# Optimization experiments

Measured on AMD Instinct MI355X. Metric: run time of the kernel, lower is better.

## Reference

```python
import jax, jax.numpy as jnp
import numpy as np


def setup_inputs() -> dict:
    key = jax.random.key(0)
    ks = jax.random.split(key, 20)
    B, T, E, U, D, O = 64, 2048, 256, 256, 256, 32000
    s = lambda k, shp, fan: (jax.random.normal(k, shp, jnp.float32) * (1.0 / np.sqrt(fan)))
    return {
        'inputs': jax.random.normal(ks[0], (B, D), jnp.float32),
        'stm': jax.random.normal(ks[1], (B, U), jnp.float32),
        'x_seq': jax.random.normal(ks[2], (B, T, E), jnp.float32),
        'V_a': s(ks[3], (U + E,), U + E),
        'W_a': s(ks[4], (U + E, U + E), U + E),
        'W_r': s(ks[5], (D, U), D), 'U_r': s(ks[6], (U, U), U), 'C_r': s(ks[7], (E, U), E), 'b_r': jnp.zeros((U,), jnp.float32),
        'W_z': s(ks[8], (D, U), D), 'U_z': s(ks[9], (U, U), U), 'C_z': s(ks[10], (E, U), E), 'b_z': jnp.zeros((U,), jnp.float32),
        'W_p': s(ks[11], (D, U), D), 'U_p': s(ks[12], (U, U), U), 'C_p': s(ks[13], (E, U), E), 'b_p': jnp.zeros((U,), jnp.float32),
        'W_o': s(ks[14], (D, O), D), 'U_o': s(ks[15], (U, O), U), 'C_o': s(ks[16], (E, O), E), 'b_o': jnp.zeros((O,), jnp.float32),
    }


def reference(inputs, stm, x_seq, V_a, W_a,
              W_r, U_r, C_r, b_r,
              W_z, U_z, C_z, b_z,
              W_p, U_p, C_p, b_p,
              W_o, U_o, C_o, b_o):
    B, T, E = x_seq.shape
    U = stm.shape[-1]
    # Bahdanau additive attention: concat repeated state with encoder seq
    _stm = jnp.broadcast_to(stm[:, None, :], (B, T, U))          # [B,T,U]
    cat = jnp.concatenate([_stm, x_seq], axis=-1)                 # [B,T,U+E]
    et = jnp.einsum('btc,c->bt', jnp.tanh(jnp.einsum('btc,cd->btd', cat, W_a)), V_a)
    at = jax.nn.softmax(et, axis=1)                               # exp / sum over T
    context = jnp.einsum('bt,bte->be', at, x_seq)                 # [B,E]
    # GRU-style gates conditioned on input, previous state, and context
    rt = jax.nn.sigmoid(inputs @ W_r + stm @ U_r + context @ C_r + b_r)
    zt = jax.nn.sigmoid(inputs @ W_z + stm @ U_z + context @ C_z + b_z)
    s_tp = jnp.tanh(inputs @ W_p + (rt * stm) @ U_p + context @ C_p + b_p)
    st = (1.0 - zt) * stm + zt * s_tp                             # new state [B,U]
    output = jax.nn.softmax(inputs @ W_o + stm @ U_o + context @ C_o + b_o, axis=-1)  # [B,O]
    return output, st
```

## Files before the change

kernel.cpp:

```cpp
#include <hip/hip_runtime.h>
#include <hip/hip_bf16.h>

#define B_ 64
#define T_ 2048
#define E_ 256
#define U_ 256
#define O_ 32000
#define UE_ 512

typedef __attribute__((ext_vector_type(8))) short bf16x8;
typedef __attribute__((ext_vector_type(4))) float f32x4;

__device__ __forceinline__ unsigned short f2bf(float f){
  __hip_bfloat16 h = __float2bfloat16(f);
  return __builtin_bit_cast(unsigned short, h);
}
__device__ __forceinline__ unsigned pk2bf(float a, float b){
  return (unsigned)f2bf(a) | ((unsigned)f2bf(b) << 16);
}
__device__ __forceinline__ bf16x8 pack8(const float* v0, const float* v1){
  float4 x = *(const float4*)v0;
  float4 y = *(const float4*)v1;
  uint4 pk;
  pk.x = pk2bf(x.x, x.y); pk.y = pk2bf(x.z, x.w);
  pk.z = pk2bf(y.x, y.y); pk.w = pk2bf(y.z, y.w);
  return __builtin_bit_cast(bf16x8, pk);
}
__device__ __forceinline__ float ftanh(float x){
  float e = __expf(2.0f*x);
  return 1.0f - 2.0f/(e + 1.0f);
}
__device__ __forceinline__ float fsig(float x){
  return 1.0f/(1.0f + __expf(-x));
}

__global__ __launch_bounds__(256)
void prep_kernel(const float* __restrict__ Wa, const float* __restrict__ stm,
                 unsigned short* __restrict__ bpack, float* __restrict__ sp){
  if (blockIdx.x < 64){
    int idx = blockIdx.x*256 + threadIdx.x;
    int n = idx & 511;
    int ktg = idx >> 9;
    int erow = ktg * 8;
    unsigned short o[8];
#pragma unroll
    for (int i = 0; i < 8; ++i)
      o[i] = f2bf(Wa[(256 + erow + i)*512 + n]);
    uint4 v;
    v.x = (unsigned)o[0] | ((unsigned)o[1] << 16);
    v.y = (unsigned)o[2] | ((unsigned)o[3] << 16);
    v.z = (unsigned)o[4] | ((unsigned)o[5] << 16);
    v.w = (unsigned)o[6] | ((unsigned)o[7] << 16);
    ((uint4*)bpack)[idx] = v;
  } else {
    int tid = threadIdx.x;
    int w = tid >> 6, l = tid & 63, c = l & 15, g = l >> 4;
    int n0 = (blockIdx.x - 64)*64 + w*16;
    f32x4 zero = {0.f,0.f,0.f,0.f};
    f32x4 acc[4];
#pragma unroll
    for (int mt = 0; mt < 4; ++mt) acc[mt] = zero;
#pragma unroll
    for (int ks = 0; ks < 8; ++ks){
      int kg = ks*32 + 8*g;
      bf16x8 a[4];
#pragma unroll
      for (int mt = 0; mt < 4; ++mt){
        const float* ap = stm + (mt*16 + c)*256 + kg;
        a[mt] = pack8(ap, ap + 4);
      }
      const float* bpt = Wa + (size_t)kg*512 + n0 + c;
      float bv[8];
#pragma unroll
      for (int i = 0; i < 8; ++i) bv[i] = bpt[(size_t)i*512];
      uint4 pk;
      pk.x = pk2bf(bv[0], bv[1]); pk.y = pk2bf(bv[2], bv[3]);
      pk.z = pk2bf(bv[4], bv[5]); pk.w = pk2bf(bv[6], bv[7]);
      bf16x8 bfr = __builtin_bit_cast(bf16x8, pk);
#pragma unroll
      for (int mt = 0; mt < 4; ++mt)
        acc[mt] = __builtin_amdgcn_mfma_f32_16x16x32_bf16(a[mt], bfr, acc[mt], 0, 0, 0);
    }
#pragma unroll
    for (int mt = 0; mt < 4; ++mt)
#pragma unroll
      for (int r = 0; r < 4; ++r){
        int m = mt*16 + 4*g + r;
        sp[m*512 + n0 + c] = acc[mt][r];
      }
  }
}

__global__ __launch_bounds__(512, 4)
void et_flash_kernel(const float* __restrict__ xseq, const unsigned short* __restrict__ bpack,
                     const float* __restrict__ va, const float* __restrict__ sp,
                     float* __restrict__ msbuf, float* __restrict__ uctxp){
  __shared__ __align__(16) uint4 sA4[2048];
  __shared__ float sVa[512];
  __shared__ float sSp[512];
  __shared__ float sEt[8][64];
  __shared__ float sE[64];
  int tid = threadIdx.x;
  int w = tid >> 6, l = tid & 63, c = l & 15, g = l >> 4;
  int m0 = blockIdx.x * 64;
  int b  = m0 >> 11;

  const float4* x4 = (const float4*)xseq + (size_t)m0 * 64;
  uint2* sA2 = (uint2*)sA4;
#pragma unroll
  for (int i = 0; i < 8; ++i){
    int p = i*512 + tid;
    int row = p >> 6, kq = p & 63;
    float4 v = x4[row*64 + kq];
    uint2 u;
    u.x = pk2bf(v.x, v.y);
    u.y = pk2bf(v.z, v.w);
    int s = ((row>>4)*8 + (kq>>3))*64 + ((kq>>1)&3)*16 + (row&15);
    sA2[(s ^ ((s>>4)&7))*2 + (kq&1)] = u;
  }
  sVa[tid] = va[tid];
  sSp[tid] = sp[b*512 + tid];
  __syncthreads();

  f32x4 zero = {0.f, 0.f, 0.f, 0.f};
  f32x4 acc[4][4];
#pragma unroll
  for (int mt = 0; mt < 4; ++mt)
#pragma unroll
    for (int tc = 0; tc < 4; ++tc) acc[mt][tc] = zero;

  const bf16x8* bp = (const bf16x8*)bpack;
#pragma unroll
  for (int ks = 0; ks < 8; ++ks){
    bf16x8 aw[4], bx[4];
    int bbase = (ks*4 + g)*512 + w*64 + c;
#pragma unroll
    for (int mt = 0; mt < 4; ++mt)
      aw[mt] = bp[bbase + mt*16];
#pragma unroll
    for (int tc = 0; tc < 4; ++tc){
      int idx = (tc*8 + ks)*64 + l;
      bx[tc] = *(const bf16x8*)&sA4[idx ^ ((idx>>4)&7)];
    }
    __builtin_amdgcn_s_setprio(1);
#pragma unroll
    for (int mt = 0; mt < 4; ++mt)
#pragma unroll
      for (int tc = 0; tc < 4; ++tc)
        acc[mt][tc] = __builtin_amdgcn_mfma_f32_16x16x32_bf16(aw[mt], bx[tc], acc[mt][tc], 0, 0, 0);
    __builtin_amdgcn_s_setprio(0);
  }

  float p[4] = {0.f, 0.f, 0.f, 0.f};
#pragma unroll
  for (int mt = 0; mt < 4; ++mt){
    int nb = w*64 + mt*16 + 4*g;
    float4 vav = *(const float4*)&sVa[nb];
    float4 spv = *(const float4*)&sSp[nb];
#pragma unroll
    for (int tc = 0; tc < 4; ++tc){
#pragma unroll
      for (int r = 0; r < 4; ++r){
        float vv = acc[mt][tc][r] + ((const float*)&spv)[r];
        p[tc] += ((const float*)&vav)[r] * ftanh(vv);
      }
    }
  }
#pragma unroll
  for (int tc = 0; tc < 4; ++tc){
    p[tc] += __shfl_xor(p[tc], 16, 64);
    p[tc] += __shfl_xor(p[tc], 32, 64);
  }
  if (l < 16){
#pragma unroll
    for (int tc = 0; tc < 4; ++tc)
      sEt[w][tc*16 + c] = p[tc];
  }
  __syncthreads();

  if (tid < 64){
    float e = 0.f;
#pragma unroll
    for (int ww = 0; ww < 8; ++ww) e += sEt[ww][tid];
    float m = e;
#pragma unroll
    for (int off = 1; off < 64; off <<= 1) m = fmaxf(m, __shfl_xor(m, off, 64));
    float ex = __expf(e - m);
    float s = ex;
#pragma unroll
    for (int off = 1; off < 64; off <<= 1) s += __shfl_xor(s, off, 64);
    sE[tid] = ex;
    if (tid == 0){
      msbuf[blockIdx.x*2]     = m;
      msbuf[blockIdx.x*2 + 1] = s;
    }
  }
  __syncthreads();

  {
    int e = tid & 255, th = tid >> 8;
    int ks = e >> 5, gg = (e >> 3) & 3, ii = e & 7;
    const unsigned short* sU = (const unsigned short*)sA4;
    float a0 = 0.f;
#pragma unroll
    for (int tt = 0; tt < 32; ++tt){
      int t = th*32 + tt;
      int mt = t >> 4, cc = t & 15;
      int slt = (mt*8 + ks)*64 + gg*16 + cc;
      unsigned short hv = sU[(size_t)(slt ^ ((slt>>4)&7))*8 + ii];
      float xv = __builtin_bit_cast(float, ((unsigned)hv) << 16);
      a0 += sE[t] * xv;
    }
    uctxp[((size_t)blockIdx.x*2 + th)*256 + e] = a0;
  }
}

__global__ void ctx_x1_kernel(const float* __restrict__ msbuf, const float* __restrict__ uctxp,
                              const float* __restrict__ inputs, const float* __restrict__ stm,
                              unsigned short* __restrict__ X1bf){
  int b = blockIdx.x, e = threadIdx.x;
  float M = -INFINITY;
#pragma unroll 4
  for (int j = 0; j < 32; ++j) M = fmaxf(M, msbuf[(32*b + j)*2]);
  float S = 0.f;
  float acc = 0.f;
#pragma unroll 4
  for (int j = 0; j < 32; ++j){
    float wj = __expf(msbuf[(32*b + j)*2] - M);
    S += msbuf[(32*b + j)*2 + 1] * wj;
    size_t base = ((size_t)(32*b + j)*2)*256 + e;
    acc += (uctxp[base] + uctxp[base + 256]) * wj;
  }
  float ctx = acc / S;
  X1bf[b*768 + e]        = f2bf(inputs[b*256 + e]);
  X1bf[b*768 + 256 + e]  = f2bf(stm[b*256 + e]);
  X1bf[b*768 + 512 + e]  = f2bf(ctx);
}

__global__ __launch_bounds__(256)
void gates1_kernel(const unsigned short* __restrict__ X1bf, const float* __restrict__ stm,
                   const float* __restrict__ Wr, const float* __restrict__ Ur,
                   const float* __restrict__ Cr, const float* __restrict__ brr,
                   const float* __restrict__ Wz, const float* __restrict__ Uz,
                   const float* __restrict__ Cz, const float* __restrict__ bzz,
                   const float* __restrict__ Wp, const float* __restrict__ Cp,
                   const float* __restrict__ bpp,
                   float* __restrict__ rs, float* __restrict__ ztb, float* __restrict__ pic){
  int tid = threadIdx.x;
  int w = tid >> 6, l = tid & 63, c = l & 15, g = l >> 4;
  int n0 = blockIdx.x*64 + w*16;
  int gate = n0 >> 8;
  int col0 = n0 & 255;
  const float* W0; const float* W1; const float* W2; const float* bias;
  if (gate == 0){ W0 = Wr; W1 = Ur; W2 = Cr; bias = brr; }
  else if (gate == 1){ W0 = Wz; W1 = Uz; W2 = Cz; bias = bzz; }
  else { W0 = Wp; W1 = nullptr; W2 = Cp; bias = bpp; }

  f32x4 zero = {0.f,0.f,0.f,0.f};
  f32x4 acc[4];
#pragma unroll
  for (int mt = 0; mt < 4; ++mt) acc[mt] = zero;

#pragma unroll
  for (int ph = 0; ph < 3; ++ph){
    const float* src = (ph == 0) ? W0 : (ph == 1) ? W1 : W2;
    if (src == nullptr) continue;
#pragma unroll
    for (int ks = 0; ks < 8; ++ks){
      int kg = ks*32 + 8*g;
      bf16x8 a[4];
#pragma unroll
      for (int mt = 0; mt < 4; ++mt)
        a[mt] = *(const bf16x8*)&X1bf[(mt*16 + c)*768 + ph*256 + kg];
      const float* bpt = src + (size_t)kg*256 + col0 + c;
      float bv[8];
#pragma unroll
      for (int i = 0; i < 8; ++i) bv[i] = bpt[(size_t)i*256];
      uint4 pk;
      pk.x = pk2bf(bv[0], bv[1]); pk.y = pk2bf(bv[2], bv[3]);
      pk.z = pk2bf(bv[4], bv[5]); pk.w = pk2bf(bv[6], bv[7]);
      bf16x8 bfr = __builtin_bit_cast(bf16x8, pk);
#pragma unroll
      for (int mt = 0; mt < 4; ++mt)
        acc[mt] = __builtin_amdgcn_mfma_f32_16x16x32_bf16(a[mt], bfr, acc[mt], 0, 0, 0);
    }
  }

  int n = col0 + c;
  float bi = bias[n];
#pragma unroll
  for (int mt = 0; mt < 4; ++mt)
#pragma unroll
    for (int r = 0; r < 4; ++r){
      int m = mt*16 + 4*g + r;
      float pre = acc[mt][r] + bi;
      if (gate == 0)      rs[m*256 + n]  = fsig(pre) * stm[m*256 + n];
      else if (gate == 1) ztb[m*256 + n] = fsig(pre);
      else                pic[m*256 + n] = pre;
    }
}

__global__ __launch_bounds__(256)
void gates2_kernel(const float* __restrict__ rs, const float* __restrict__ Up,
                   const float* __restrict__ pic, const float* __restrict__ ztb,
                   const float* __restrict__ stm, float* __restrict__ stout){
  int tid = threadIdx.x;
  int w = tid >> 6, l = tid & 63, c = l & 15, g = l >> 4;
  int n0 = blockIdx.x*64 + w*16;
  f32x4 zero = {0.f,0.f,0.f,0.f};
  f32x4 acc[4];
#pragma unroll
  for (int mt = 0; mt < 4; ++mt) acc[mt] = zero;
#pragma unroll
  for (int ks = 0; ks < 8; ++ks){
    int kg = ks*32 + 8*g;
    bf16x8 a[4];
#pragma unroll
    for (int mt = 0; mt < 4; ++mt){
      const float* ap = rs + (mt*16 + c)*256 + kg;
      a[mt] = pack8(ap, ap + 4);
    }
    const float* bpt = Up + (size_t)kg*256 + n0 + c;
    float bv[8];
#pragma unroll
    for (int i = 0; i < 8; ++i) bv[i] = bpt[(size_t)i*256];
    uint4 pk;
    pk.x = pk2bf(bv[0], bv[1]); pk.y = pk2bf(bv[2], bv[3]);
    pk.z = pk2bf(bv[4], bv[5]); pk.w = pk2bf(bv[6], bv[7]);
    bf16x8 bfr = __builtin_bit_cast(bf16x8, pk);
#pragma unroll
    for (int mt = 0; mt < 4; ++mt)
      acc[mt] = __builtin_amdgcn_mfma_f32_16x16x32_bf16(a[mt], bfr, acc[mt], 0, 0, 0);
  }
#pragma unroll
  for (int mt = 0; mt < 4; ++mt)
#pragma unroll
    for (int r = 0; r < 4; ++r){
      int m = mt*16 + 4*g + r;
      int o = m*256 + n0 + c;
      float ap = pic[o] + acc[mt][r];
      float z = ztb[o];
      stout[o] = (1.f - z)*stm[o] + z*ftanh(ap);
    }
}

__global__ __launch_bounds__(512)
void logits_mfma_kernel(const unsigned short* __restrict__ X1bf,
                        const float* __restrict__ Wo, const float* __restrict__ Uo,
                        const float* __restrict__ Co, const float* __restrict__ boo,
                        float* __restrict__ outl, float* __restrict__ part2){
  __shared__ float sAcc[16][4][64];
  __shared__ float sMx[4][64];
  __shared__ float sSx[4][64];
  int tid = threadIdx.x;
  int w = tid >> 6, l = tid & 63, c = l & 15, g = l >> 4;
  int wc = w & 3;
  int kh = w >> 2;
  int n0 = blockIdx.x*64 + wc*16;
  f32x4 zero = {0.f,0.f,0.f,0.f};
  f32x4 acc[4];
#pragma unroll
  for (int mt = 0; mt < 4; ++mt) acc[mt] = zero;

#pragma unroll
  for (int ph = 0; ph < 3; ++ph){
    const float* src = (ph == 0) ? Wo : (ph == 1) ? Uo : Co;
#pragma unroll
    for (int kss = 0; kss < 4; ++kss){
      int ks = 2*kss + kh;
      int kg = ph*256 + ks*32 + 8*g;
      bf16x8 a[4];
#pragma unroll
      for (int mt = 0; mt < 4; ++mt)
        a[mt] = *(const bf16x8*)&X1bf[(mt*16 + c)*768 + kg];
      const float* bpt = src + (size_t)(ks*32 + 8*g)*32000 + n0 + c;
      float bv[8];
#pragma unroll
      for (int i = 0; i < 8; ++i) bv[i] = bpt[(size_t)i*32000];
      uint4 pk;
      pk.x = pk2bf(bv[0], bv[1]);
      pk.y = pk2bf(bv[2], bv[3]);
      pk.z = pk2bf(bv[4], bv[5]);
      pk.w = pk2bf(bv[6], bv[7]);
      bf16x8 bfr = __builtin_bit_cast(bf16x8, pk);
#pragma unroll
      for (int mt = 0; mt < 4; ++mt)
        acc[mt] = __builtin_amdgcn_mfma_f32_16x16x32_bf16(a[mt], bfr, acc[mt], 0, 0, 0);
    }
  }

  if (kh == 1){
#pragma unroll
    for (int mt = 0; mt < 4; ++mt)
#pragma unroll
      for (int r = 0; r < 4; ++r)
        sAcc[mt*4 + r][wc][l] = acc[mt][r];
  }
  __syncthreads();

  bool active = (kh == 0);
  float vv[4][4];
  if (active){
    float bias = boo[n0 + c];
#pragma unroll
    for (int mt = 0; mt < 4; ++mt)
#pragma unroll
      for (int r = 0; r < 4; ++r){
        int m = mt*16 + 4*g + r;
        vv[mt][r] = acc[mt][r] + sAcc[mt*4 + r][wc][l] + bias;
        outl[(size_t)m*32000 + n0 + c] = vv[mt][r];
      }
    float mx[4][4];
#pragma unroll
    for (int mt = 0; mt < 4; ++mt)
#pragma unroll
      for (int r = 0; r < 4; ++r) mx[mt][r] = vv[mt][r];
#pragma unroll
    for (int mask = 1; mask < 16; mask <<= 1)
#pragma unroll
      for (int mt = 0; mt < 4; ++mt)
#pragma unroll
        for (int r = 0; r < 4; ++r)
          mx[mt][r] = fmaxf(mx[mt][r], __shfl_xor(mx[mt][r], mask, 64));
    if (c == 0)
#pragma unroll
      for (int mt = 0; mt < 4; ++mt)
#pragma unroll
        for (int r = 0; r < 4; ++r)
          sMx[wc][mt*16 + 4*g + r] = mx[mt][r];
  }
  __syncthreads();
  if (active){
    float sx[4][4];
#pragma unroll
    for (int mt = 0; mt < 4; ++mt)
#pragma unroll
      for (int r = 0; r < 4; ++r){
        int row = mt*16 + 4*g + r;
        float M = fmaxf(fmaxf(sMx[0][row], sMx[1][row]), fmaxf(sMx[2][row], sMx[3][row]));
        sx[mt][r] = __expf(vv[mt][r] - M);
      }
#pragma unroll
    for (int mask = 1; mask < 16; mask <<= 1)
#pragma unroll
      for (int mt = 0; mt < 4; ++mt)
#pragma unroll
        for (int r = 0; r < 4; ++r)
          sx[mt][r] += __shfl_xor(sx[mt][r], mask, 64);
    if (c == 0)
#pragma unroll
      for (int mt = 0; mt < 4; ++mt)
#pragma unroll
        for (int r = 0; r < 4; ++r)
          sSx[wc][mt*16 + 4*g + r] = sx[mt][r];
  }
  __syncthreads();
  if (tid < 64){
    int row = tid;
    float M = fmaxf(fmaxf(sMx[0][row], sMx[1][row]), fmaxf(sMx[2][row], sMx[3][row]));
    float S = sSx[0][row] + sSx[1][row] + sSx[2][row] + sSx[3][row];
    part2[((size_t)blockIdx.x*64 + row)*2]     = M;
    part2[((size_t)blockIdx.x*64 + row)*2 + 1] = S;
  }
}

__global__ __launch_bounds__(512)
void sm_norm_kernel(float* __restrict__ logits, const float* __restrict__ part2){
  __shared__ float red[8];
  __shared__ float red2[8];
  __shared__ float sMS[2];
  int bid = blockIdx.x;
  int b = bid >> 3, ch = bid & 7;
  int base = b*32000 + ch*4000;
  int tid = threadIdx.x;

  float M = -INFINITY, S = 0.f;
  if (tid < 500){
    M = part2[((size_t)tid*64 + b)*2];
    S = part2[((size_t)tid*64 + b)*2 + 1];
  }
  float m1 = M;
#pragma unroll
  for (int off = 1; off < 64; off <<= 1) m1 = fmaxf(m1, __shfl_xor(m1, off, 64));
  int wv = tid >> 6;
  if ((tid & 63) == 0) red[wv] = m1;
  __syncthreads();
  float Mg = red[0];
#pragma unroll
  for (int i = 1; i < 8; ++i) Mg = fmaxf(Mg, red[i]);
  float s1 = (tid < 500) ? S * __expf(M - Mg) : 0.f;
#pragma unroll
  for (int off = 1; off < 64; off <<= 1) s1 += __shfl_xor(s1, off, 64);
  if ((tid & 63) == 0) red2[wv] = s1;
  __syncthreads();
  if (tid == 0){
    float St = 0.f;
#pragma unroll
    for (int i = 0; i < 8; ++i) St += red2[i];
    sMS[0] = Mg;
    sMS[1] = 1.0f / St;
  }
  __syncthreads();
  float Mf = sMS[0];
  float inv = sMS[1];
#pragma unroll
  for (int i = 0; i < 8; ++i){
    int idx = i*512 + tid;
    if (idx < 4000){
      int o = base + idx;
      logits[o] = __expf(logits[o] - Mf) * inv;
    }
  }
}

extern "C" void kernel_launch(void* const* d_in, const int* in_sizes, int n_in,
                              void* d_out, int out_size, void* d_ws, size_t ws_size,
                              hipStream_t stream) {
  const float* inputs = (const float*)d_in[0];
  const float* stm    = (const float*)d_in[1];
  const float* xseq   = (const float*)d_in[2];
  const float* Va     = (const float*)d_in[3];
  const float* Wa     = (const float*)d_in[4];
  const float* Wr = (const float*)d_in[5];
  const float* Ur = (const float*)d_in[6];
  const float* Cr = (const float*)d_in[7];
  const float* br = (const float*)d_in[8];
  const float* Wz = (const float*)d_in[9];
  const float* Uz = (const float*)d_in[10];
  const float* Cz = (const float*)d_in[11];
  const float* bz = (const float*)d_in[12];
  const float* Wp = (const float*)d_in[13];
  const float* Up = (const float*)d_in[14];
  const float* Cp = (const float*)d_in[15];
  const float* bp = (const float*)d_in[16];
  const float* Wo = (const float*)d_in[17];
  const float* Uo = (const float*)d_in[18];
  const float* Co = (const float*)d_in[19];
  const float* bo = (const float*)d_in[20];

  float* out   = (float*)d_out;
  float* stout = out + (size_t)B_*O_;

  float* wsf = (float*)d_ws;
  unsigned short* bpack = (unsigned short*)d_ws;
  float* sp    = wsf + 65536;
  float* msbuf = wsf + 98304;
  float* uctxp = wsf + 102400;
  float* part2 = wsf + 102400;
  unsigned short* X1bf = (unsigned short*)(wsf + 1150976);
  float* rs    = wsf + 1176576;
  float* ztb   = wsf + 1192960;
  float* pic   = wsf + 1209344;

  prep_kernel<<<72, 256, 0, stream>>>(Wa, stm, bpack, sp);
  et_flash_kernel<<<2048, 512, 0, stream>>>(xseq, bpack, Va, sp, msbuf, uctxp);
  ctx_x1_kernel<<<64, 256, 0, stream>>>(msbuf, uctxp, inputs, stm, X1bf);
  gates1_kernel<<<12, 256, 0, stream>>>(X1bf, stm, Wr, Ur, Cr, br,
                                        Wz, Uz, Cz, bz, Wp, Cp, bp,
                                        rs, ztb, pic);
  gates2_kernel<<<4, 256, 0, stream>>>(rs, Up, pic, ztb, stm, stout);
  logits_mfma_kernel<<<500, 512, 0, stream>>>(X1bf, Wo, Uo, Co, bo, out, part2);
  sm_norm_kernel<<<512, 512, 0, stream>>>(out, part2);
}
```

Before: 161.3 us.

## Overlap context-independent logits GEMM with attention kernel via extra blocks

Splits the output-logits GEMM so the inputs·W_o and stm·U_o parts, which don't depend on the attention context, run as extra blocks appended to the attention kernel launch. The final logits kernel now only multiplies the context by C_o and adds the stored partial sums. The bf16 packing of inputs and stm moves into the prep kernel so it is ready earlier. The goal is to hide logits weight streaming behind the x_seq pass. The cost is writing and reading back an extra full-size partial-logit buffer, plus contention between the two workloads.

```diff
diff --git a/kernel.cpp b/kernel.cpp
--- a/kernel.cpp
+++ b/kernel.cpp
@@ -36,7 +36,9 @@
 
 __global__ __launch_bounds__(256)
 void prep_kernel(const float* __restrict__ Wa, const float* __restrict__ stm,
-                 unsigned short* __restrict__ bpack, float* __restrict__ sp){
+                 const float* __restrict__ inputs,
+                 unsigned short* __restrict__ bpack, float* __restrict__ sp,
+                 unsigned short* __restrict__ X1bf){
   if (blockIdx.x < 64){
     int idx = blockIdx.x*256 + threadIdx.x;
     int n = idx & 511;
@@ -52,7 +54,7 @@
     v.z = (unsigned)o[4] | ((unsigned)o[5] << 16);
     v.w = (unsigned)o[6] | ((unsigned)o[7] << 16);
     ((uint4*)bpack)[idx] = v;
-  } else {
+  } else if (blockIdx.x < 72){
     int tid = threadIdx.x;
     int w = tid >> 6, l = tid & 63, c = l & 15, g = l >> 4;
     int n0 = (blockIdx.x - 64)*64 + w*16;
@@ -88,19 +90,84 @@
         int m = mt*16 + 4*g + r;
         sp[m*512 + n0 + c] = acc[mt][r];
       }
+  } else {
+    for (int j = threadIdx.x; j < 32768; j += 256){
+      int b = j >> 9, col = j & 511;
+      float v = (col < 256) ? inputs[b*256 + col] : stm[b*256 + col - 256];
+      X1bf[b*768 + col] = f2bf(v);
+    }
   }
 }
 
 __global__ __launch_bounds__(512, 4)
 void et_flash_kernel(const float* __restrict__ xseq, const unsigned short* __restrict__ bpack,
                      const float* __restrict__ va, const float* __restrict__ sp,
-                     float* __restrict__ msbuf, float* __restrict__ uctxp){
+                     float* __restrict__ msbuf, float* __restrict__ uctxp,
+                     const unsigned short* __restrict__ X1bf,
+                     const float* __restrict__ Wo, const float* __restrict__ Uo,
+                     float* __restrict__ lpart){
   __shared__ __align__(16) uint4 sA4[2048];
   __shared__ float sVa[512];
   __shared__ float sSp[512];
   __shared__ float sEt[8][64];
   __shared__ float sE[64];
   int tid = threadIdx.x;
+
+  if (blockIdx.x >= 2048){
+    int pb = blockIdx.x - 2048;
+    int w = tid >> 6, l = tid & 63, c = l & 15, g = l >> 4;
+    int wc = w & 3;
+    int kh = w >> 2;
+    int n0 = pb*64 + wc*16;
+    float* sAcc = (float*)sA4;
+    f32x4 zero = {0.f,0.f,0.f,0.f};
+    f32x4 acc[4];
+#pragma unroll
+    for (int mt = 0; mt < 4; ++mt) acc[mt] = zero;
+#pragma unroll
+    for (int ph = 0; ph < 2; ++ph){
+      const float* src = (ph == 0) ? Wo : Uo;
+#pragma unroll
+      for (int kss = 0; kss < 4; ++kss){
+        int ks = 2*kss + kh;
+        int kg = ph*256 + ks*32 + 8*g;
+        bf16x8 a[4];
+#pragma unroll
+        for (int mt = 0; mt < 4; ++mt)
+          a[mt] = *(const bf16x8*)&X1bf[(mt*16 + c)*768 + kg];
+        const float* bpt = src + (size_t)(ks*32 + 8*g)*32000 + n0 + c;
+        float bv[8];
+#pragma unroll
+        for (int i = 0; i < 8; ++i) bv[i] = bpt[(size_t)i*32000];
+        uint4 pk;
+        pk.x = pk2bf(bv[0], bv[1]); pk.y = pk2bf(bv[2], bv[3]);
+        pk.z = pk2bf(bv[4], bv[5]); pk.w = pk2bf(bv[6], bv[7]);
+        bf16x8 bfr = __builtin_bit_cast(bf16x8, pk);
+#pragma unroll
+        for (int mt = 0; mt < 4; ++mt)
+          acc[mt] = __builtin_amdgcn_mfma_f32_16x16x32_bf16(a[mt], bfr, acc[mt], 0, 0, 0);
+      }
+    }
+    if (kh == 1){
+#pragma unroll
+      for (int mt = 0; mt < 4; ++mt)
+#pragma unroll
+        for (int r = 0; r < 4; ++r)
+          sAcc[(mt*4 + r)*256 + wc*64 + l] = acc[mt][r];
+    }
+    __syncthreads();
+    if (kh == 0){
+#pragma unroll
+      for (int mt = 0; mt < 4; ++mt)
+#pragma unroll
+        for (int r = 0; r < 4; ++r){
+          int m = mt*16 + 4*g + r;
+          lpart[(size_t)m*32000 + n0 + c] = acc[mt][r] + sAcc[(mt*4 + r)*256 + wc*64 + l];
+        }
+    }
+    return;
+  }
+
   int w = tid >> 6, l = tid & 63, c = l & 15, g = l >> 4;
   int m0 = blockIdx.x * 64;
   int b  = m0 >> 11;
@@ -216,7 +283,6 @@
 }
 
 __global__ void ctx_x1_kernel(const float* __restrict__ msbuf, const float* __restrict__ uctxp,
-                              const float* __restrict__ inputs, const float* __restrict__ stm,
                               unsigned short* __restrict__ X1bf){
   int b = blockIdx.x, e = threadIdx.x;
   float M = -INFINITY;
@@ -232,9 +298,7 @@
     acc += (uctxp[base] + uctxp[base + 256]) * wj;
   }
   float ctx = acc / S;
-  X1bf[b*768 + e]        = f2bf(inputs[b*256 + e]);
-  X1bf[b*768 + 256 + e]  = f2bf(stm[b*256 + e]);
-  X1bf[b*768 + 512 + e]  = f2bf(ctx);
+  X1bf[b*768 + 512 + e] = f2bf(ctx);
 }
 
 __global__ __launch_bounds__(256)
@@ -345,10 +409,10 @@
 }
 
 __global__ __launch_bounds__(512)
-void logits_mfma_kernel(const unsigned short* __restrict__ X1bf,
-                        const float* __restrict__ Wo, const float* __restrict__ Uo,
-                        const float* __restrict__ Co, const float* __restrict__ boo,
-                        float* __restrict__ outl, float* __restrict__ part2){
+void logits_final_kernel(const unsigned short* __restrict__ X1bf,
+                         const float* __restrict__ Co, const float* __restrict__ lpart,
+                         const float* __restrict__ boo,
+                         float* __restrict__ outl, float* __restrict__ part2){
   __shared__ float sAcc[16][4][64];
   __shared__ float sMx[4][64];
   __shared__ float sSx[4][64];
@@ -363,30 +427,26 @@
   for (int mt = 0; mt < 4; ++mt) acc[mt] = zero;
 
 #pragma unroll
-  for (int ph = 0; ph < 3; ++ph){
-    const float* src = (ph == 0) ? Wo : (ph == 1) ? Uo : Co;
-#pragma unroll
-    for (int kss = 0; kss < 4; ++kss){
-      int ks = 2*kss + kh;
-      int kg = ph*256 + ks*32 + 8*g;
-      bf16x8 a[4];
-#pragma unroll
-      for (int mt = 0; mt < 4; ++mt)
-        a[mt] = *(const bf16x8*)&X1bf[(mt*16 + c)*768 + kg];
-      const float* bpt = src + (size_t)(ks*32 + 8*g)*32000 + n0 + c;
-      float bv[8];
-#pragma unroll
-      for (int i = 0; i < 8; ++i) bv[i] = bpt[(size_t)i*32000];
-      uint4 pk;
-      pk.x = pk2bf(bv[0], bv[1]);
-      pk.y = pk2bf(bv[2], bv[3]);
-      pk.z = pk2bf(bv[4], bv[5]);
-      pk.w = pk2bf(bv[6], bv[7]);
-      bf16x8 bfr = __builtin_bit_cast(bf16x8, pk);
-#pragma unroll
-      for (int mt = 0; mt < 4; ++mt)
-        acc[mt] = __builtin_amdgcn_mfma_f32_16x16x32_bf16(a[mt], bfr, acc[mt], 0, 0, 0);
-    }
+  for (int kss = 0; kss < 4; ++kss){
+    int ks = 2*kss + kh;
+    int kg = 512 + ks*32 + 8*g;
+    bf16x8 a[4];
+#pragma unroll
+    for (int mt = 0; mt < 4; ++mt)
+      a[mt] = *(const bf16x8*)&X1bf[(mt*16 + c)*768 + kg];
+    const float* bpt = Co + (size_t)(ks*32 + 8*g)*32000 + n0 + c;
+    float bv[8];
+#pragma unroll
+    for (int i = 0; i < 8; ++i) bv[i] = bpt[(size_t)i*32000];
+    uint4 pk;
+    pk.x = pk2bf(bv[0], bv[1]);
+    pk.y = pk2bf(bv[2], bv[3]);
+    pk.z = pk2bf(bv[4], bv[5]);
+    pk.w = pk2bf(bv[6], bv[7]);
+    bf16x8 bfr = __builtin_bit_cast(bf16x8, pk);
+#pragma unroll
+    for (int mt = 0; mt < 4; ++mt)
+      acc[mt] = __builtin_amdgcn_mfma_f32_16x16x32_bf16(a[mt], bfr, acc[mt], 0, 0, 0);
   }
 
   if (kh == 1){
@@ -407,7 +467,7 @@
 #pragma unroll
       for (int r = 0; r < 4; ++r){
         int m = mt*16 + 4*g + r;
-        vv[mt][r] = acc[mt][r] + sAcc[mt*4 + r][wc][l] + bias;
+        vv[mt][r] = acc[mt][r] + sAcc[mt*4 + r][wc][l] + lpart[(size_t)m*32000 + n0 + c] + bias;
         outl[(size_t)m*32000 + n0 + c] = vv[mt][r];
       }
     float mx[4][4];
@@ -551,14 +611,16 @@
   float* rs    = wsf + 1176576;
   float* ztb   = wsf + 1192960;
   float* pic   = wsf + 1209344;
-
-  prep_kernel<<<72, 256, 0, stream>>>(Wa, stm, bpack, sp);
-  et_flash_kernel<<<2048, 512, 0, stream>>>(xseq, bpack, Va, sp, msbuf, uctxp);
-  ctx_x1_kernel<<<64, 256, 0, stream>>>(msbuf, uctxp, inputs, stm, X1bf);
+  float* lpart = wsf + 1225728;
+
+  prep_kernel<<<73, 256, 0, stream>>>(Wa, stm, inputs, bpack, sp, X1bf);
+  et_flash_kernel<<<2548, 512, 0, stream>>>(xseq, bpack, Va, sp, msbuf, uctxp,
+                                            X1bf, Wo, Uo, lpart);
+  ctx_x1_kernel<<<64, 256, 0, stream>>>(msbuf, uctxp, X1bf);
   gates1_kernel<<<12, 256, 0, stream>>>(X1bf, stm, Wr, Ur, Cr, br,
                                         Wz, Uz, Cz, bz, Wp, Cp, bp,
                                         rs, ztb, pic);
   gates2_kernel<<<4, 256, 0, stream>>>(rs, Up, pic, ztb, stm, stout);
-  logits_mfma_kernel<<<500, 512, 0, stream>>>(X1bf, Wo, Uo, Co, bo, out, part2);
+  logits_final_kernel<<<500, 512, 0, stream>>>(X1bf, Co, lpart, bo, out, part2);
   sm_norm_kernel<<<512, 512, 0, stream>>>(out, part2);
 }
```

Measured after the change: 174.5 us. 1.08x slower.
